# Optimization experiments

Hardware: AMD Instinct MI355X
Metric: run time of the kernel (lower is better)

Reference implementation:

```python
import jax, jax.numpy as jnp
import numpy as np

EMBED_DIM = 1024
NUM_HEADS = 16
HEAD_DIM = EMBED_DIM // NUM_HEADS
TGT_LEN = 2048
BSZ = 2
NEG_INF = -1e30  # stand-in for float('-inf') masked_fill, safe under fp16/bf16 via dtype min below


def setup_inputs() -> dict:
    key = jax.random.key(0)
    ks = jax.random.split(key, 12)
    wscale = 1.0 / np.sqrt(EMBED_DIM)  # keep logits in a sane range
    return {
        "query": jax.random.normal(ks[0], (TGT_LEN, BSZ, EMBED_DIM), jnp.float32),
        "key_padding_mask": jax.random.randint(ks[1], (BSZ, TGT_LEN), 0, 2).astype(jnp.bool_),
        "attn_qw": jax.random.normal(ks[2], (EMBED_DIM, EMBED_DIM), jnp.float32) * wscale,
        "attn_qb": jax.random.normal(ks[3], (EMBED_DIM,), jnp.float32) * wscale,
        "attn_kw": jax.random.normal(ks[4], (EMBED_DIM, EMBED_DIM), jnp.float32) * wscale,
        "attn_kb": jax.random.normal(ks[5], (EMBED_DIM,), jnp.float32) * wscale,
        "attn_vw": jax.random.normal(ks[6], (EMBED_DIM, EMBED_DIM), jnp.float32) * wscale,
        "attn_vb": jax.random.normal(ks[7], (EMBED_DIM,), jnp.float32) * wscale,
        "attn_ow": jax.random.normal(ks[8], (EMBED_DIM, EMBED_DIM), jnp.float32) * wscale,
        "attn_ob": jax.random.normal(ks[9], (EMBED_DIM,), jnp.float32) * wscale,
    }


def _mha(query, key_padding_mask, qw, qb, kw, kb, vw, vb, ow, ob):
    tgt_len, bsz, embed_dim = query.shape
    scaling = HEAD_DIM ** (-0.5)
    # self-attention projections: F.linear(x, W, b) == x @ W.T + b
    q = (query @ qw.T + qb) * scaling
    k = query @ kw.T + kb
    v = query @ vw.T + vb
    # (tgt, bsz, E) -> (bsz*H, tgt, hd)
    def to_bh(x):
        return x.reshape(tgt_len, bsz * NUM_HEADS, HEAD_DIM).transpose(1, 0, 2)
    q, k, v = to_bh(q), to_bh(k), to_bh(v)
    src_len = k.shape[1]
    # scores: (bsz*H, tgt, src)
    attn_weights = jnp.einsum('bqd,bkd->bqk', q, k)
    # padding mask: True -> -inf, broadcast over heads and query positions
    mask = key_padding_mask[:, None, None, :]  # (bsz, 1, 1, src)
    attn_weights = attn_weights.reshape(bsz, NUM_HEADS, tgt_len, src_len)
    attn_weights = jnp.where(mask, jnp.finfo(attn_weights.dtype).min, attn_weights)
    attn_weights = attn_weights.reshape(bsz * NUM_HEADS, tgt_len, src_len)
    attn_weights = jax.nn.softmax(attn_weights, axis=-1)
    attn = jnp.einsum('bqk,bkd->bqd', attn_weights, v)  # (bsz*H, tgt, hd)
    attn = attn.transpose(1, 0, 2).reshape(tgt_len, bsz, embed_dim)
    attn = attn @ ow.T + ob
    return attn, attn_weights


def reference(query, key_padding_mask, attn_qw, attn_qb, attn_kw, attn_kb,
              attn_vw, attn_vb, attn_ow, attn_ob):
    return _mha(query, key_padding_mask, attn_qw, attn_qb, attn_kw, attn_kb,
                attn_vw, attn_vb, attn_ow, attn_ob)
```

## Files before the change

kernel.cpp:

```cpp
#include <hip/hip_runtime.h>
#include <cstdint>
#include <cstddef>

#define TGT  2048
#define BSZN 2
#define NH   16
#define HD   64
#define ED   1024
#define ROWS (TGT*BSZN)
#define BHN  (BSZN*NH)

typedef __attribute__((ext_vector_type(8))) short short8;
typedef __attribute__((ext_vector_type(4))) float floatx4;

__device__ inline unsigned short f2bf(float f) {
    unsigned u = __float_as_uint(f);
    u += 0x7FFFu + ((u >> 16) & 1u);
    return (unsigned short)(u >> 16);
}
__device__ inline float bf2f(unsigned short s) {
    return __uint_as_float(((unsigned)s) << 16);
}

__global__ __launch_bounds__(256) void prep_mask(const unsigned char* __restrict__ mraw,
                                                 float* __restrict__ maskf) {
    __shared__ int cf, cb;
    int tid = threadIdx.x;
    if (tid == 0) { cf = 0; cb = 0; }
    __syncthreads();
    int lf = 0, lb = 0;
    for (int i = tid; i < BSZN * TGT; i += 256) {
        unsigned char v = mraw[i];
        if ((i & 3) == 3 && v == 0x3F) lf++;
        if ((i & 3) != 0 && v != 0)    lb++;
    }
    if (lf) atomicAdd(&cf, lf);
    if (lb) atomicAdd(&cb, lb);
    __syncthreads();
    int fmt = (cf > 256) ? 2 : (cb > 0 ? 1 : 0);
    for (int i = tid; i < BSZN * TGT; i += 256) {
        bool on;
        if (fmt == 2)      on = ((const float*)mraw)[i] != 0.0f;
        else if (fmt == 1) on = (mraw[i] != 0);
        else               on = (mraw[4 * i] != 0);
        maskf[i] = on ? 1.0f : 0.0f;
    }
}

__global__ __launch_bounds__(256) void convert_hilo(const float* __restrict__ src,
                                                    unsigned short* __restrict__ dh,
                                                    unsigned short* __restrict__ dl,
                                                    int n4) {
    int i = blockIdx.x * 256 + threadIdx.x;
    if (i >= n4) return;
    float4 v = ((const float4*)src)[i];
    ushort4 h, l;
    h.x = f2bf(v.x); l.x = f2bf(v.x - bf2f(h.x));
    h.y = f2bf(v.y); l.y = f2bf(v.y - bf2f(h.y));
    h.z = f2bf(v.z); l.z = f2bf(v.z - bf2f(h.z));
    h.w = f2bf(v.w); l.w = f2bf(v.w - bf2f(h.w));
    ((ushort4*)dh)[i] = h;
    ((ushort4*)dl)[i] = l;
}

__global__ __launch_bounds__(256) void gemm_split(
    const unsigned short* __restrict__ AH, const unsigned short* __restrict__ AL,
    const unsigned short* __restrict__ BH, const unsigned short* __restrict__ BL,
    const float* __restrict__ bias, float scale, int K,
    int mode, float* __restrict__ Yf, unsigned short* __restrict__ Yb, int ldy)
{
    __shared__ unsigned short Ahs[128][72];
    __shared__ unsigned short Als[128][72];
    __shared__ unsigned short Bhs[64][72];
    __shared__ unsigned short Bls[64][72];

    int tid = threadIdx.x;
    int w = tid >> 6, lane = tid & 63, lm = lane & 15, quad = lane >> 4;
    int m0 = blockIdx.y * 128, n0 = blockIdx.x * 64;

    floatx4 acc[2][4];
#pragma unroll
    for (int g = 0; g < 2; ++g)
#pragma unroll
        for (int j = 0; j < 4; ++j) acc[g][j] = (floatx4){0.f, 0.f, 0.f, 0.f};

    for (int kt = 0; kt < K; kt += 64) {
#pragma unroll
        for (int s = 0; s < 4; ++s) {
            int idx = tid + s * 256;
            int r = idx >> 3, c8 = (idx & 7) * 8;
            *(short8*)&Ahs[r][c8] = *(const short8*)&AH[(size_t)(m0 + r) * ED + kt + c8];
            *(short8*)&Als[r][c8] = *(const short8*)&AL[(size_t)(m0 + r) * ED + kt + c8];
        }
#pragma unroll
        for (int s = 0; s < 2; ++s) {
            int idx = tid + s * 256;
            int r = idx >> 3, c8 = (idx & 7) * 8;
            *(short8*)&Bhs[r][c8] = *(const short8*)&BH[(size_t)(n0 + r) * ED + kt + c8];
            *(short8*)&Bls[r][c8] = *(const short8*)&BL[(size_t)(n0 + r) * ED + kt + c8];
        }
        __syncthreads();
#pragma unroll
        for (int kk = 0; kk < 64; kk += 32) {
            short8 ah0 = *(const short8*)&Ahs[w * 32 + lm][kk + quad * 8];
            short8 al0 = *(const short8*)&Als[w * 32 + lm][kk + quad * 8];
            short8 ah1 = *(const short8*)&Ahs[w * 32 + 16 + lm][kk + quad * 8];
            short8 al1 = *(const short8*)&Als[w * 32 + 16 + lm][kk + quad * 8];
#pragma unroll
            for (int j = 0; j < 4; ++j) {
                short8 bh = *(const short8*)&Bhs[j * 16 + lm][kk + quad * 8];
                short8 bl = *(const short8*)&Bls[j * 16 + lm][kk + quad * 8];
                floatx4 t0 = acc[0][j];
                t0 = __builtin_amdgcn_mfma_f32_16x16x32_bf16(ah0, bl, t0, 0, 0, 0);
                t0 = __builtin_amdgcn_mfma_f32_16x16x32_bf16(al0, bh, t0, 0, 0, 0);
                t0 = __builtin_amdgcn_mfma_f32_16x16x32_bf16(ah0, bh, t0, 0, 0, 0);
                acc[0][j] = t0;
                floatx4 t1 = acc[1][j];
                t1 = __builtin_amdgcn_mfma_f32_16x16x32_bf16(ah1, bl, t1, 0, 0, 0);
                t1 = __builtin_amdgcn_mfma_f32_16x16x32_bf16(al1, bh, t1, 0, 0, 0);
                t1 = __builtin_amdgcn_mfma_f32_16x16x32_bf16(ah1, bh, t1, 0, 0, 0);
                acc[1][j] = t1;
            }
        }
        __syncthreads();
    }

    if (mode == 2) {
        unsigned short (*Ct)[72] = Ahs;
#pragma unroll
        for (int g = 0; g < 2; ++g)
#pragma unroll
            for (int j = 0; j < 4; ++j)
#pragma unroll
                for (int r = 0; r < 4; ++r) {
                    int row = w * 32 + g * 16 + quad * 4 + r;
                    int col = j * 16 + lm;
                    Ct[row][col] = f2bf(acc[g][j][r] + bias[n0 + col]);
                }
        __syncthreads();
        int h = n0 >> 6;
        int seg = tid >> 1, half = tid & 1;
        int bsel = seg >> 6, d = seg & 63;
        size_t base = ((size_t)((bsel * NH + h) * HD + d)) * TGT + (m0 >> 1) + half * 32;
#pragma unroll
        for (int grp = 0; grp < 4; ++grp) {
            short8 ov;
#pragma unroll
            for (int u = 0; u < 8; ++u) {
                int tl = half * 32 + grp * 8 + u;
                ov[u] = (short)Ct[tl * 2 + bsel][d];
            }
            *(short8*)&Yb[base + grp * 8] = ov;
        }
    } else {
#pragma unroll
        for (int g = 0; g < 2; ++g)
#pragma unroll
            for (int j = 0; j < 4; ++j)
#pragma unroll
                for (int r = 0; r < 4; ++r) {
                    int grow = m0 + w * 32 + g * 16 + quad * 4 + r;
                    int col = n0 + j * 16 + lm;
                    float val = (acc[g][j][r] + bias[col]) * scale;
                    if (mode == 0) Yf[(size_t)grow * ldy + col] = val;
                    else           Yb[(size_t)grow * ldy + col] = f2bf(val);
                }
    }
}

__global__ __launch_bounds__(256) void scores_pv_fused(
    const unsigned short* __restrict__ qH, const unsigned short* __restrict__ kH,
    const unsigned short* __restrict__ vT, const float* __restrict__ maskf,
    float* __restrict__ wout,
    unsigned short* __restrict__ ctxH, unsigned short* __restrict__ ctxL)
{
    __shared__ float ot[4][16][68];
    __shared__ float rsx[4][4][4];
    int tid = threadIdx.x;
    int w = tid >> 6, lane = tid & 63, lm = lane & 15, quad = lane >> 4;
    int rg = w >> 1, half = w & 1;

    int slot = blockIdx.x;
    int xcd = slot & 7, rr = slot >> 3;
    int bh = xcd * 4 + (rr >> 6);
    int t0 = (rr & 63) * 32;
    int bsel = bh >> 4, h = bh & 15;
    int k0 = half * (TGT / 2);

    const unsigned short* qrow =
        qH + ((size_t)((t0 + rg * 16 + lm) * BSZN + bsel)) * ED + h * HD + quad * 8;
    short8 a0 = *(const short8*)qrow;
    short8 a1 = *(const short8*)(qrow + 32);

    const float* mrow = maskf + bsel * TGT;
    float* wbh = wout + (size_t)bh * TGT * TGT;
    const unsigned short* vb = vT + (size_t)bh * HD * TGT;

    float rs[4] = {0.f, 0.f, 0.f, 0.f};
    for (int s0 = k0; s0 < k0 + TGT / 2; s0 += 32) {
        int keyA = s0 + lm, keyB = s0 + 16 + lm;
        const unsigned short* krA = kH + ((size_t)(keyA * BSZN + bsel)) * ED + h * HD + quad * 8;
        const unsigned short* krB = kH + ((size_t)(keyB * BSZN + bsel)) * ED + h * HD + quad * 8;
        short8 b0A = *(const short8*)krA;
        short8 b1A = *(const short8*)(krA + 32);
        short8 b0B = *(const short8*)krB;
        short8 b1B = *(const short8*)(krB + 32);
        float mkA = mrow[keyA], mkB = mrow[keyB];
        floatx4 sA = (floatx4){0.f, 0.f, 0.f, 0.f};
        floatx4 sB = (floatx4){0.f, 0.f, 0.f, 0.f};
        sA = __builtin_amdgcn_mfma_f32_16x16x32_bf16(a0, b0A, sA, 0, 0, 0);
        sB = __builtin_amdgcn_mfma_f32_16x16x32_bf16(a0, b0B, sB, 0, 0, 0);
        sA = __builtin_amdgcn_mfma_f32_16x16x32_bf16(a1, b1A, sA, 0, 0, 0);
        sB = __builtin_amdgcn_mfma_f32_16x16x32_bf16(a1, b1B, sB, 0, 0, 0);
#pragma unroll
        for (int r = 0; r < 4; ++r) {
            rs[r] += (mkA != 0.f) ? 0.f : __expf(sA[r]);
            rs[r] += (mkB != 0.f) ? 0.f : __expf(sB[r]);
        }
    }
#pragma unroll
    for (int off = 1; off < 16; off <<= 1) {
#pragma unroll
        for (int r = 0; r < 4; ++r) rs[r] += __shfl_xor(rs[r], off, 64);
    }
    if (lm == 0) {
#pragma unroll
        for (int r = 0; r < 4; ++r) rsx[w][quad][r] = rs[r];
    }
    __syncthreads();
    float rinv[4];
#pragma unroll
    for (int r = 0; r < 4; ++r) rinv[r] = 1.0f / (rs[r] + rsx[w ^ 1][quad][r]);

    floatx4 acc[4];
#pragma unroll
    for (int j = 0; j < 4; ++j) acc[j] = (floatx4){0.f, 0.f, 0.f, 0.f};

    float* wrow = wbh + (size_t)(t0 + rg * 16 + quad * 4) * TGT;

    for (int c0 = k0; c0 < k0 + TGT / 2; c0 += 64) {
#pragma unroll
        for (int sub = 0; sub < 4; ++sub) {
            int key = c0 + sub * 16 + lm;
            const unsigned short* kr = kH + ((size_t)(key * BSZN + bsel)) * ED + h * HD + quad * 8;
            short8 b0 = *(const short8*)kr;
            short8 b1 = *(const short8*)(kr + 32);
            floatx4 s = (floatx4){0.f, 0.f, 0.f, 0.f};
            s = __builtin_amdgcn_mfma_f32_16x16x32_bf16(a0, b0, s, 0, 0, 0);
            s = __builtin_amdgcn_mfma_f32_16x16x32_bf16(a1, b1, s, 0, 0, 0);
            float mk = mrow[key];
#pragma unroll
            for (int r = 0; r < 4; ++r) {
                float e = (mk != 0.f) ? 0.f : __expf(s[r]);
                float v = e * rinv[r];
                __builtin_nontemporal_store(v, &wrow[(size_t)r * TGT + key]);
                ot[w][quad * 4 + r][sub * 16 + lm] = v;
            }
        }
#pragma unroll
        for (int kk = 0; kk < 64; kk += 32) {
            const float* pr = &ot[w][lm][kk + quad * 8];
            float4 p0 = *(const float4*)pr;
            float4 p1 = *(const float4*)(pr + 4);
            short8 af;
            af[0] = (short)f2bf(p0.x); af[1] = (short)f2bf(p0.y);
            af[2] = (short)f2bf(p0.z); af[3] = (short)f2bf(p0.w);
            af[4] = (short)f2bf(p1.x); af[5] = (short)f2bf(p1.y);
            af[6] = (short)f2bf(p1.z); af[7] = (short)f2bf(p1.w);
#pragma unroll
            for (int j = 0; j < 4; ++j) {
                short8 bf = *(const short8*)&vb[(size_t)(j * 16 + lm) * TGT + c0 + kk + quad * 8];
                acc[j] = __builtin_amdgcn_mfma_f32_16x16x32_bf16(af, bf, acc[j], 0, 0, 0);
            }
        }
    }

    if (half) {
#pragma unroll
        for (int j = 0; j < 4; ++j)
#pragma unroll
            for (int r = 0; r < 4; ++r)
                ot[w][quad * 4 + r][j * 16 + lm] = acc[j][r];
    }
    __syncthreads();
    if (!half) {
#pragma unroll
        for (int j = 0; j < 4; ++j)
#pragma unroll
            for (int r = 0; r < 4; ++r)
                acc[j][r] += ot[w + 1][quad * 4 + r][j * 16 + lm];

#pragma unroll
        for (int j = 0; j < 4; ++j)
#pragma unroll
            for (int r = 0; r < 4; ++r) {
                int t = t0 + rg * 16 + quad * 4 + r;
                int d = j * 16 + lm;
                size_t idx = (size_t)(t * BSZN + bsel) * ED + h * HD + d;
                float val = acc[j][r];
                unsigned short hi = f2bf(val);
                ctxH[idx] = hi;
                ctxL[idx] = f2bf(val - bf2f(hi));
            }
    }
}

extern "C" void kernel_launch(void* const* d_in, const int* in_sizes, int n_in,
                              void* d_out, int out_size, void* d_ws, size_t ws_size,
                              hipStream_t stream) {
    const float* query = (const float*)d_in[0];
    const unsigned char* mraw = (const unsigned char*)d_in[1];
    const float* qw = (const float*)d_in[2];
    const float* qb = (const float*)d_in[3];
    const float* kw = (const float*)d_in[4];
    const float* kb = (const float*)d_in[5];
    const float* vw = (const float*)d_in[6];
    const float* vb = (const float*)d_in[7];
    const float* ow = (const float*)d_in[8];
    const float* ob = (const float*)d_in[9];

    float* out  = (float*)d_out;
    float* wout = out + (size_t)ROWS * ED;

    char* wsb = (char*)d_ws;
    float* maskf           = (float*)(wsb);
    unsigned short* qryH   = (unsigned short*)(wsb + 65536);
    unsigned short* qryL   = qryH + (size_t)ROWS * ED;
    unsigned short* wWH    = qryL + (size_t)ROWS * ED;
    unsigned short* wWL    = wWH + (size_t)ED * ED;
    unsigned short* qHp    = wWL + (size_t)ED * ED;
    unsigned short* kHp    = qHp + (size_t)ROWS * ED;
    unsigned short* vT     = kHp + (size_t)ROWS * ED;
    unsigned short* ctxH   = qryH;
    unsigned short* ctxL   = qryL;

    dim3 blk(256);
    dim3 ggrid(ED / 64, ROWS / 128);

    prep_mask<<<1, blk, 0, stream>>>(mraw, maskf);
    convert_hilo<<<(ROWS * ED / 4 + 255) / 256, blk, 0, stream>>>(query, qryH, qryL, ROWS * ED / 4);

    convert_hilo<<<(ED * ED / 4 + 255) / 256, blk, 0, stream>>>(qw, wWH, wWL, ED * ED / 4);
    gemm_split<<<ggrid, blk, 0, stream>>>(qryH, qryL, wWH, wWL, qb, 0.125f, ED, 1, nullptr, qHp, ED);
    convert_hilo<<<(ED * ED / 4 + 255) / 256, blk, 0, stream>>>(kw, wWH, wWL, ED * ED / 4);
    gemm_split<<<ggrid, blk, 0, stream>>>(qryH, qryL, wWH, wWL, kb, 1.0f, ED, 1, nullptr, kHp, ED);
    convert_hilo<<<(ED * ED / 4 + 255) / 256, blk, 0, stream>>>(vw, wWH, wWL, ED * ED / 4);
    gemm_split<<<ggrid, blk, 0, stream>>>(qryH, qryL, wWH, wWL, vb, 1.0f, ED, 2, nullptr, vT, ED);

    scores_pv_fused<<<dim3(BHN * (TGT / 32)), blk, 0, stream>>>(qHp, kHp, vT, maskf, wout, ctxH, ctxL);

    convert_hilo<<<(ED * ED / 4 + 255) / 256, blk, 0, stream>>>(ow, wWH, wWL, ED * ED / 4);
    gemm_split<<<ggrid, blk, 0, stream>>>(ctxH, ctxL, wWH, wWL, ob, 1.0f, ED, 0, out, nullptr, ED);
}
```

Measured before the change: 1.009 ms.

## Shrink attention blocks to 16 rows and store probabilities as bf16 in LDS

The fused scores/PV kernel now uses 128-thread blocks, each covering 16 query rows with two waves splitting the key range, and launches twice as many blocks. Probabilities are converted to bf16 before they go to shared memory, which halves LDS use and drops the per-kk conversion. The attention-weight stores change from nontemporal to ordinary stores. More, smaller blocks may raise occupancy, at the cost of loading K and V once per 16 rows instead of once per 32.

```diff
diff --git a/kernel.cpp b/kernel.cpp
--- a/kernel.cpp
+++ b/kernel.cpp
@@ -168,27 +168,26 @@
     }
 }
 
-__global__ __launch_bounds__(256) void scores_pv_fused(
+__global__ __launch_bounds__(128) void scores_pv_fused(
     const unsigned short* __restrict__ qH, const unsigned short* __restrict__ kH,
     const unsigned short* __restrict__ vT, const float* __restrict__ maskf,
     float* __restrict__ wout,
     unsigned short* __restrict__ ctxH, unsigned short* __restrict__ ctxL)
 {
-    __shared__ float ot[4][16][68];
-    __shared__ float rsx[4][4][4];
+    __shared__ unsigned short ot[2][16][72];
+    __shared__ float rsx[2][4][4];
     int tid = threadIdx.x;
     int w = tid >> 6, lane = tid & 63, lm = lane & 15, quad = lane >> 4;
-    int rg = w >> 1, half = w & 1;
 
     int slot = blockIdx.x;
     int xcd = slot & 7, rr = slot >> 3;
-    int bh = xcd * 4 + (rr >> 6);
-    int t0 = (rr & 63) * 32;
+    int bh = xcd * 4 + (rr >> 7);
+    int t0 = (rr & 127) * 16;
     int bsel = bh >> 4, h = bh & 15;
-    int k0 = half * (TGT / 2);
+    int k0 = w * (TGT / 2);
 
     const unsigned short* qrow =
-        qH + ((size_t)((t0 + rg * 16 + lm) * BSZN + bsel)) * ED + h * HD + quad * 8;
+        qH + ((size_t)((t0 + lm) * BSZN + bsel)) * ED + h * HD + quad * 8;
     short8 a0 = *(const short8*)qrow;
     short8 a1 = *(const short8*)(qrow + 32);
 
@@ -236,7 +235,7 @@
 #pragma unroll
     for (int j = 0; j < 4; ++j) acc[j] = (floatx4){0.f, 0.f, 0.f, 0.f};
 
-    float* wrow = wbh + (size_t)(t0 + rg * 16 + quad * 4) * TGT;
+    float* wrow = wbh + (size_t)(t0 + quad * 4) * TGT;
 
     for (int c0 = k0; c0 < k0 + TGT / 2; c0 += 64) {
 #pragma unroll
@@ -253,20 +252,13 @@
             for (int r = 0; r < 4; ++r) {
                 float e = (mk != 0.f) ? 0.f : __expf(s[r]);
                 float v = e * rinv[r];
-                __builtin_nontemporal_store(v, &wrow[(size_t)r * TGT + key]);
-                ot[w][quad * 4 + r][sub * 16 + lm] = v;
+                wrow[(size_t)r * TGT + key] = v;
+                ot[w][quad * 4 + r][sub * 16 + lm] = f2bf(v);
             }
         }
 #pragma unroll
         for (int kk = 0; kk < 64; kk += 32) {
-            const float* pr = &ot[w][lm][kk + quad * 8];
-            float4 p0 = *(const float4*)pr;
-            float4 p1 = *(const float4*)(pr + 4);
-            short8 af;
-            af[0] = (short)f2bf(p0.x); af[1] = (short)f2bf(p0.y);
-            af[2] = (short)f2bf(p0.z); af[3] = (short)f2bf(p0.w);
-            af[4] = (short)f2bf(p1.x); af[5] = (short)f2bf(p1.y);
-            af[6] = (short)f2bf(p1.z); af[7] = (short)f2bf(p1.w);
+            short8 af = *(const short8*)&ot[w][lm][kk + quad * 8];
 #pragma unroll
             for (int j = 0; j < 4; ++j) {
                 short8 bf = *(const short8*)&vb[(size_t)(j * 16 + lm) * TGT + c0 + kk + quad * 8];
@@ -275,26 +267,28 @@
         }
     }
 
-    if (half) {
+    float* cmb = (float*)&ot[0][0][0];
+    __syncthreads();
+    if (w == 1) {
 #pragma unroll
         for (int j = 0; j < 4; ++j)
 #pragma unroll
             for (int r = 0; r < 4; ++r)
-                ot[w][quad * 4 + r][j * 16 + lm] = acc[j][r];
-    }
-    __syncthreads();
-    if (!half) {
+                cmb[(quad * 4 + r) * 68 + j * 16 + lm] = acc[j][r];
+    }
+    __syncthreads();
+    if (w == 0) {
 #pragma unroll
         for (int j = 0; j < 4; ++j)
 #pragma unroll
             for (int r = 0; r < 4; ++r)
-                acc[j][r] += ot[w + 1][quad * 4 + r][j * 16 + lm];
+                acc[j][r] += cmb[(quad * 4 + r) * 68 + j * 16 + lm];
 
 #pragma unroll
         for (int j = 0; j < 4; ++j)
 #pragma unroll
             for (int r = 0; r < 4; ++r) {
-                int t = t0 + rg * 16 + quad * 4 + r;
+                int t = t0 + quad * 4 + r;
                 int d = j * 16 + lm;
                 size_t idx = (size_t)(t * BSZN + bsel) * ED + h * HD + d;
                 float val = acc[j][r];
@@ -347,7 +341,7 @@
     convert_hilo<<<(ED * ED / 4 + 255) / 256, blk, 0, stream>>>(vw, wWH, wWL, ED * ED / 4);
     gemm_split<<<ggrid, blk, 0, stream>>>(qryH, qryL, wWH, wWL, vb, 1.0f, ED, 2, nullptr, vT, ED);
 
-    scores_pv_fused<<<dim3(BHN * (TGT / 32)), blk, 0, stream>>>(qHp, kHp, vT, maskf, wout, ctxH, ctxL);
+    scores_pv_fused<<<dim3(BHN * (TGT / 16)), dim3(128), 0, stream>>>(qHp, kHp, vT, maskf, wout, ctxH, ctxL);
 
     convert_hilo<<<(ED * ED / 4 + 255) / 256, blk, 0, stream>>>(ow, wWH, wWL, ED * ED / 4);
     gemm_split<<<ggrid, blk, 0, stream>>>(ctxH, ctxL, wWH, wWL, ob, 1.0f, ED, 0, out, nullptr, ED);
```

New measurement: 1.047 ms. +3.8%, slower.

## Store K and V in MFMA fragment-packed layouts for contiguous per-lane loads

Applied to the files above, without the earlier changes.

The K and V projection epilogues now write per-head tiles pre-swizzled into the MFMA operand layout, so each lane in the attention kernel reads 16 contiguous bytes from one dense 1KB block instead of strided rows. The probability staging buffer in shared memory now holds bf16 instead of fp32, which removes the conversion step on reload and halves LDS traffic. Attention-weight stores switch from nontemporal to normal stores. In exchange, the K epilogue does scattered 2-byte global writes, which may make that GEMM slower.

```diff
diff --git a/kernel.cpp b/kernel.cpp
--- a/kernel.cpp
+++ b/kernel.cpp
@@ -138,20 +138,43 @@
                     Ct[row][col] = f2bf(acc[g][j][r] + bias[n0 + col]);
                 }
         __syncthreads();
-        int h = n0 >> 6;
-        int seg = tid >> 1, half = tid & 1;
-        int bsel = seg >> 6, d = seg & 63;
-        size_t base = ((size_t)((bsel * NH + h) * HD + d)) * TGT + (m0 >> 1) + half * 32;
+        int hh = n0 >> 6;
+        int seg = tid >> 1, hf = tid & 1;
+        int bsel2 = seg >> 6, dd = seg & 63;
+        int bhx = bsel2 * 16 + hh;
+        size_t bhbase = (size_t)bhx * HD * TGT;
 #pragma unroll
         for (int grp = 0; grp < 4; ++grp) {
+            int key0 = (m0 >> 1) + hf * 32 + grp * 8;
+            size_t base = bhbase + (size_t)(key0 >> 5) * 2048 + (size_t)(dd >> 4) * 512
+                        + (size_t)((key0 >> 3) & 3) * 128 + (size_t)(dd & 15) * 8;
             short8 ov;
 #pragma unroll
             for (int u = 0; u < 8; ++u) {
-                int tl = half * 32 + grp * 8 + u;
-                ov[u] = (short)Ct[tl * 2 + bsel][d];
-            }
-            *(short8*)&Yb[base + grp * 8] = ov;
-        }
+                int tl = hf * 32 + grp * 8 + u;
+                ov[u] = (short)Ct[tl * 2 + bsel2][dd];
+            }
+            *(short8*)&Yb[base] = ov;
+        }
+    } else if (mode == 3) {
+        int hh = n0 >> 6;
+#pragma unroll
+        for (int g = 0; g < 2; ++g)
+#pragma unroll
+            for (int j = 0; j < 4; ++j)
+#pragma unroll
+                for (int r = 0; r < 4; ++r) {
+                    int grow = m0 + w * 32 + g * 16 + quad * 4 + r;
+                    int col = n0 + j * 16 + lm;
+                    int t = grow >> 1, b = grow & 1;
+                    int d = col & 63;
+                    int bhx = b * 16 + hh;
+                    float val = (acc[g][j][r] + bias[col]) * scale;
+                    size_t a = (size_t)bhx * TGT * HD + (size_t)(t >> 4) * 1024
+                             + (size_t)(d >> 5) * 512 + (size_t)((d >> 3) & 3) * 128
+                             + (size_t)(t & 15) * 8 + (size_t)(d & 7);
+                    Yb[a] = f2bf(val);
+                }
     } else {
 #pragma unroll
         for (int g = 0; g < 2; ++g)
@@ -169,12 +192,12 @@
 }
 
 __global__ __launch_bounds__(256) void scores_pv_fused(
-    const unsigned short* __restrict__ qH, const unsigned short* __restrict__ kH,
-    const unsigned short* __restrict__ vT, const float* __restrict__ maskf,
+    const unsigned short* __restrict__ qH, const unsigned short* __restrict__ kT,
+    const unsigned short* __restrict__ vTt, const float* __restrict__ maskf,
     float* __restrict__ wout,
     unsigned short* __restrict__ ctxH, unsigned short* __restrict__ ctxL)
 {
-    __shared__ float ot[4][16][68];
+    __shared__ unsigned short ot[4][16][72];
     __shared__ float rsx[4][4][4];
     int tid = threadIdx.x;
     int w = tid >> 6, lane = tid & 63, lm = lane & 15, quad = lane >> 4;
@@ -192,20 +215,21 @@
     short8 a0 = *(const short8*)qrow;
     short8 a1 = *(const short8*)(qrow + 32);
 
+    const unsigned short* kbh = kT + (size_t)bh * TGT * HD;
+    const unsigned short* vbh = vTt + (size_t)bh * HD * TGT;
     const float* mrow = maskf + bsel * TGT;
     float* wbh = wout + (size_t)bh * TGT * TGT;
-    const unsigned short* vb = vT + (size_t)bh * HD * TGT;
 
     float rs[4] = {0.f, 0.f, 0.f, 0.f};
     for (int s0 = k0; s0 < k0 + TGT / 2; s0 += 32) {
-        int keyA = s0 + lm, keyB = s0 + 16 + lm;
-        const unsigned short* krA = kH + ((size_t)(keyA * BSZN + bsel)) * ED + h * HD + quad * 8;
-        const unsigned short* krB = kH + ((size_t)(keyB * BSZN + bsel)) * ED + h * HD + quad * 8;
-        short8 b0A = *(const short8*)krA;
-        short8 b1A = *(const short8*)(krA + 32);
-        short8 b0B = *(const short8*)krB;
-        short8 b1B = *(const short8*)(krB + 32);
-        float mkA = mrow[keyA], mkB = mrow[keyB];
+        int cA = s0 >> 4;
+        const unsigned short* pA = kbh + (size_t)cA * 1024 + lane * 8;
+        const unsigned short* pB = pA + 1024;
+        short8 b0A = *(const short8*)pA;
+        short8 b1A = *(const short8*)(pA + 512);
+        short8 b0B = *(const short8*)pB;
+        short8 b1B = *(const short8*)(pB + 512);
+        float mkA = mrow[s0 + lm], mkB = mrow[s0 + 16 + lm];
         floatx4 sA = (floatx4){0.f, 0.f, 0.f, 0.f};
         floatx4 sB = (floatx4){0.f, 0.f, 0.f, 0.f};
         sA = __builtin_amdgcn_mfma_f32_16x16x32_bf16(a0, b0A, sA, 0, 0, 0);
@@ -241,10 +265,11 @@
     for (int c0 = k0; c0 < k0 + TGT / 2; c0 += 64) {
 #pragma unroll
         for (int sub = 0; sub < 4; ++sub) {
+            int c = (c0 >> 4) + sub;
+            const unsigned short* p = kbh + (size_t)c * 1024 + lane * 8;
+            short8 b0 = *(const short8*)p;
+            short8 b1 = *(const short8*)(p + 512);
             int key = c0 + sub * 16 + lm;
-            const unsigned short* kr = kH + ((size_t)(key * BSZN + bsel)) * ED + h * HD + quad * 8;
-            short8 b0 = *(const short8*)kr;
-            short8 b1 = *(const short8*)(kr + 32);
             floatx4 s = (floatx4){0.f, 0.f, 0.f, 0.f};
             s = __builtin_amdgcn_mfma_f32_16x16x32_bf16(a0, b0, s, 0, 0, 0);
             s = __builtin_amdgcn_mfma_f32_16x16x32_bf16(a1, b1, s, 0, 0, 0);
@@ -253,34 +278,30 @@
             for (int r = 0; r < 4; ++r) {
                 float e = (mk != 0.f) ? 0.f : __expf(s[r]);
                 float v = e * rinv[r];
-                __builtin_nontemporal_store(v, &wrow[(size_t)r * TGT + key]);
-                ot[w][quad * 4 + r][sub * 16 + lm] = v;
+                wrow[(size_t)r * TGT + key] = v;
+                ot[w][quad * 4 + r][sub * 16 + lm] = f2bf(v);
             }
         }
 #pragma unroll
         for (int kk = 0; kk < 64; kk += 32) {
-            const float* pr = &ot[w][lm][kk + quad * 8];
-            float4 p0 = *(const float4*)pr;
-            float4 p1 = *(const float4*)(pr + 4);
-            short8 af;
-            af[0] = (short)f2bf(p0.x); af[1] = (short)f2bf(p0.y);
-            af[2] = (short)f2bf(p0.z); af[3] = (short)f2bf(p0.w);
-            af[4] = (short)f2bf(p1.x); af[5] = (short)f2bf(p1.y);
-            af[6] = (short)f2bf(p1.z); af[7] = (short)f2bf(p1.w);
+            short8 af = *(const short8*)&ot[w][lm][kk + quad * 8];
+            size_t vbase = (size_t)((c0 + kk) >> 5) * 2048 + lane * 8;
 #pragma unroll
             for (int j = 0; j < 4; ++j) {
-                short8 bf = *(const short8*)&vb[(size_t)(j * 16 + lm) * TGT + c0 + kk + quad * 8];
+                short8 bf = *(const short8*)&vbh[vbase + (size_t)j * 512];
                 acc[j] = __builtin_amdgcn_mfma_f32_16x16x32_bf16(af, bf, acc[j], 0, 0, 0);
             }
         }
     }
 
+    float* cmb = (float*)&ot[rg * 2][0][0];
+    __syncthreads();
     if (half) {
 #pragma unroll
         for (int j = 0; j < 4; ++j)
 #pragma unroll
             for (int r = 0; r < 4; ++r)
-                ot[w][quad * 4 + r][j * 16 + lm] = acc[j][r];
+                cmb[(quad * 4 + r) * 68 + j * 16 + lm] = acc[j][r];
     }
     __syncthreads();
     if (!half) {
@@ -288,7 +309,7 @@
         for (int j = 0; j < 4; ++j)
 #pragma unroll
             for (int r = 0; r < 4; ++r)
-                acc[j][r] += ot[w + 1][quad * 4 + r][j * 16 + lm];
+                acc[j][r] += cmb[(quad * 4 + r) * 68 + j * 16 + lm];
 
 #pragma unroll
         for (int j = 0; j < 4; ++j)
@@ -329,8 +350,8 @@
     unsigned short* wWH    = qryL + (size_t)ROWS * ED;
     unsigned short* wWL    = wWH + (size_t)ED * ED;
     unsigned short* qHp    = wWL + (size_t)ED * ED;
-    unsigned short* kHp    = qHp + (size_t)ROWS * ED;
-    unsigned short* vT     = kHp + (size_t)ROWS * ED;
+    unsigned short* kTt    = qHp + (size_t)ROWS * ED;
+    unsigned short* vTt    = kTt + (size_t)ROWS * ED;
     unsigned short* ctxH   = qryH;
     unsigned short* ctxL   = qryL;
 
@@ -343,11 +364,11 @@
     convert_hilo<<<(ED * ED / 4 + 255) / 256, blk, 0, stream>>>(qw, wWH, wWL, ED * ED / 4);
     gemm_split<<<ggrid, blk, 0, stream>>>(qryH, qryL, wWH, wWL, qb, 0.125f, ED, 1, nullptr, qHp, ED);
     convert_hilo<<<(ED * ED / 4 + 255) / 256, blk, 0, stream>>>(kw, wWH, wWL, ED * ED / 4);
-    gemm_split<<<ggrid, blk, 0, stream>>>(qryH, qryL, wWH, wWL, kb, 1.0f, ED, 1, nullptr, kHp, ED);
+    gemm_split<<<ggrid, blk, 0, stream>>>(qryH, qryL, wWH, wWL, kb, 1.0f, ED, 3, nullptr, kTt, ED);
     convert_hilo<<<(ED * ED / 4 + 255) / 256, blk, 0, stream>>>(vw, wWH, wWL, ED * ED / 4);
-    gemm_split<<<ggrid, blk, 0, stream>>>(qryH, qryL, wWH, wWL, vb, 1.0f, ED, 2, nullptr, vT, ED);
-
-    scores_pv_fused<<<dim3(BHN * (TGT / 32)), blk, 0, stream>>>(qHp, kHp, vT, maskf, wout, ctxH, ctxL);
+    gemm_split<<<ggrid, blk, 0, stream>>>(qryH, qryL, wWH, wWL, vb, 1.0f, ED, 2, nullptr, vTt, ED);
+
+    scores_pv_fused<<<dim3(BHN * (TGT / 32)), blk, 0, stream>>>(qHp, kTt, vTt, maskf, wout, ctxH, ctxL);
 
     convert_hilo<<<(ED * ED / 4 + 255) / 256, blk, 0, stream>>>(ow, wWH, wWL, ED * ED / 4);
     gemm_split<<<ggrid, blk, 0, stream>>>(ctxH, ctxL, wWH, wWL, ob, 1.0f, ED, 0, out, nullptr, ED);
```

Result: faster. 844.5 us (-16.3%).
